# Kernel tuning notes

Hardware: AMD Instinct MI355X
Metric: run time of the kernel (lower is better)

The kernel has to match this reference:

```python
import jax, jax.numpy as jnp
import numpy as np

HEADS = 8
DIM_HEAD = 128
ATTN_MATRIX_SCALE = 1.5  # tau applied to mean-centered logits
SCALE = DIM_HEAD ** -0.5


def setup_inputs() -> dict:
    key = jax.random.key(0)
    ks = jax.random.split(key, 7)
    b, n, m = 2, 2048, 2048
    qd, cd, inner = 1024, 768, HEADS * DIM_HEAD
    x = jax.random.normal(ks[0], (b, n, qd), dtype=jnp.float32)
    context = jax.random.normal(ks[1], (b, m, cd), dtype=jnp.float32)
    Wq = jax.random.normal(ks[2], (qd, inner), dtype=jnp.float32) * (qd ** -0.5)
    Wk = jax.random.normal(ks[3], (cd, inner), dtype=jnp.float32) * (cd ** -0.5)
    Wv = jax.random.normal(ks[4], (cd, inner), dtype=jnp.float32) * (cd ** -0.5)
    Wout = jax.random.normal(ks[5], (inner, qd), dtype=jnp.float32) * (inner ** -0.5)
    bout = jnp.zeros((qd,), dtype=jnp.float32)
    return {"x": x, "context": context, "Wq": Wq, "Wk": Wk, "Wv": Wv,
            "Wout": Wout, "bout": bout}


def _split_heads(t):
    # (b, n, h*d) -> (h, b*n, d); matches rearrange '(b h) n d -> h (b n) d'
    b, n, _ = t.shape
    t = t.reshape(b, n, HEADS, DIM_HEAD)
    return t.transpose(2, 0, 1, 3).reshape(HEADS, b * n, DIM_HEAD)


def reference(x, context, Wq, Wk, Wv, Wout, bout):
    b, n, _ = x.shape
    qh = _split_heads(jnp.einsum('bnq,qi->bni', x, Wq))        # (h, b*n, d)
    kh = _split_heads(jnp.einsum('bmc,ci->bmi', context, Wk))  # (h, b*m, d)
    vh = _split_heads(jnp.einsum('bmc,ci->bmi', context, Wv))  # (h, b*m, d)

    # custom mean-centered / tau-scaled similarity (_compute_sim_with_tau)
    sim = jnp.einsum('hid,hjd->hij', qh, kh) * SCALE
    mean = jnp.mean(sim, axis=-1, keepdims=True)
    sim = (sim - mean) * ATTN_MATRIX_SCALE + mean

    attn = jax.nn.softmax(sim, axis=-1)
    out = jnp.einsum('hij,hjd->hid', attn, vh)                 # (h, b*n, d)

    # (h, b*n, d) -> (b, n, h*d)
    out = out.reshape(HEADS, b, n, DIM_HEAD).transpose(1, 2, 0, 3)
    out = out.reshape(b, n, HEADS * DIM_HEAD)
    return jnp.einsum('bni,iq->bnq', out, Wout) + bout
```

## Files before the change

### kernel.cpp

```cpp
#include <hip/hip_runtime.h>
#include <cstdint>
#include <cstddef>

typedef unsigned short u16t;
typedef __bf16 bf16x8_t __attribute__((ext_vector_type(8)));
typedef float f32x4_t __attribute__((ext_vector_type(4)));

#define MFMA_BF16 __builtin_amdgcn_mfma_f32_16x16x32_bf16

__device__ __forceinline__ u16t f2bf(float f) {
    uint32_t u = __builtin_bit_cast(uint32_t, f);
    u += 0x7fffu + ((u >> 16) & 1u);
    return (u16t)(u >> 16);
}

__device__ __forceinline__ uint32_t pk2bf(float a, float b) {
    return (uint32_t)f2bf(a) | ((uint32_t)f2bf(b) << 16);
}

__device__ __forceinline__ uint32_t pk2bf_fast(float a, float b) {
    uint32_t au = __builtin_bit_cast(uint32_t, a) + 0x8000u;
    uint32_t bu = __builtin_bit_cast(uint32_t, b) + 0x8000u;
    return __builtin_amdgcn_perm(bu, au, 0x07060302u);
}

__device__ __forceinline__ float bflo(uint32_t u) {
    return __builtin_bit_cast(float, u << 16);
}
__device__ __forceinline__ float bfhi(uint32_t u) {
    return __builtin_bit_cast(float, u & 0xffff0000u);
}

__device__ __forceinline__ bf16x8_t ld_frag(const u16t* p) {
    return __builtin_bit_cast(bf16x8_t, *(const uint4*)p);
}

__device__ __forceinline__ void gl_lds16(const u16t* g, u16t* l) {
    __builtin_amdgcn_global_load_lds(
        (const __attribute__((address_space(1))) void*)g,
        (__attribute__((address_space(3))) void*)l, 16, 0, 0);
}

__global__ void cast2_bf16_kernel(const float* __restrict__ s0, u16t* __restrict__ d0, int n0,
                                  const float* __restrict__ s1, u16t* __restrict__ d1, int n1) {
    int i = blockIdx.x * blockDim.x + threadIdx.x;
    const float* s; u16t* d;
    if (i < n0) { s = s0; d = d0; }
    else { i -= n0; if (i >= n1) return; s = s1; d = d1; }
    float4 v = ((const float4*)s)[i];
    uint2 o;
    o.x = pk2bf(v.x, v.y);
    o.y = pk2bf(v.z, v.w);
    ((uint2*)d)[i] = o;
}

__global__ void transpose4_kernel(const float* __restrict__ Wq, const float* __restrict__ Wk,
                                  const float* __restrict__ Wv, const float* __restrict__ Wo,
                                  u16t* __restrict__ Wqt, u16t* __restrict__ Wkt,
                                  u16t* __restrict__ Wvt, u16t* __restrict__ Wot) {
    const int z = blockIdx.z;
    const float* W = z == 0 ? Wq : (z == 1 ? Wk : (z == 2 ? Wv : Wo));
    u16t* Wt      = z == 0 ? Wqt : (z == 1 ? Wkt : (z == 2 ? Wvt : Wot));
    const int K   = (z == 1 || z == 2) ? 768 : 1024;
    const int N = 1024;
    int n0 = blockIdx.x * 32, k0 = blockIdx.y * 32;
    if (k0 >= K) return;
    __shared__ float tile[32][33];
    int tx = threadIdx.x, ty = threadIdx.y;
    for (int i = ty; i < 32; i += 8)
        tile[i][tx] = W[(size_t)(k0 + i) * N + n0 + tx];
    __syncthreads();
    for (int i = ty; i < 32; i += 8)
        Wt[(size_t)(n0 + i) * K + k0 + tx] = f2bf(tile[tx][i]);
}

__device__ __forceinline__ void gemm_core(
    const u16t* __restrict__ A, const u16t* __restrict__ Bt,
    int K, void* __restrict__ outp, const float* __restrict__ bias,
    int mode, float oscale, int bm, int bn)
{
    __shared__ __align__(16) u16t As[2][128 * 64];
    __shared__ __align__(16) u16t Bs[2][64 * 64];
    const int tid = threadIdx.x;
    const int wave = tid >> 6, lane = tid & 63;
    const int wm = wave & 1, wn = wave >> 1;
    const int quad = lane >> 4, l16 = lane & 15;

    const int l8r = lane >> 3, l8c = lane & 7;
    const int cgx = (l8c ^ l8r) * 8;

    f32x4_t acc[4][2];
#pragma unroll
    for (int i = 0; i < 4; ++i)
#pragma unroll
        for (int j = 0; j < 2; ++j) acc[i][j] = (f32x4_t){0.f, 0.f, 0.f, 0.f};

    const int nk = K >> 6;

#pragma unroll
    for (int it = 0; it < 4; ++it) {
        int rb = wave * 32 + it * 8;
        gl_lds16(&A[(size_t)(bm + rb + l8r) * K + cgx], &As[0][rb * 64]);
    }
#pragma unroll
    for (int it = 0; it < 2; ++it) {
        int rb = wave * 16 + it * 8;
        gl_lds16(&Bt[(size_t)(bn + rb + l8r) * K + cgx], &Bs[0][rb * 64]);
    }

    for (int ki = 0; ki < nk; ++ki) {
        const int buf = ki & 1;
        __syncthreads();

        if (ki + 1 < nk) {
            const int kc = (ki + 1) << 6;
#pragma unroll
            for (int it = 0; it < 4; ++it) {
                int rb = wave * 32 + it * 8;
                gl_lds16(&A[(size_t)(bm + rb + l8r) * K + kc + cgx], &As[buf ^ 1][rb * 64]);
            }
#pragma unroll
            for (int it = 0; it < 2; ++it) {
                int rb = wave * 16 + it * 8;
                gl_lds16(&Bt[(size_t)(bn + rb + l8r) * K + kc + cgx], &Bs[buf ^ 1][rb * 64]);
            }
        }

#pragma unroll
        for (int ks = 0; ks < 2; ++ks) {
            bf16x8_t af[4], bfv[2];
#pragma unroll
            for (int i = 0; i < 4; ++i) {
                int r = wm * 64 + i * 16 + l16;
                af[i] = ld_frag(&As[buf][r * 64 + (((ks * 4 + quad) ^ (r & 7)) * 8)]);
            }
#pragma unroll
            for (int j = 0; j < 2; ++j) {
                int r = wn * 32 + j * 16 + l16;
                bfv[j] = ld_frag(&Bs[buf][r * 64 + (((ks * 4 + quad) ^ (r & 7)) * 8)]);
            }
#pragma unroll
            for (int i = 0; i < 4; ++i)
#pragma unroll
                for (int j = 0; j < 2; ++j)
                    acc[i][j] = MFMA_BF16(af[i], bfv[j], acc[i][j], 0, 0, 0);
        }
    }

    if (mode == 3) {
        float* out = (float*)outp;
#pragma unroll
        for (int j = 0; j < 2; ++j) {
            int c = bn + wn * 32 + j * 16 + l16;
            float b = bias[c];
#pragma unroll
            for (int i = 0; i < 4; ++i) {
                int rb = bm + wm * 64 + i * 16 + quad * 4;
#pragma unroll
                for (int r = 0; r < 4; ++r)
                    out[(size_t)(rb + r) * 1024 + c] = acc[i][j][r] + b;
            }
        }
    } else if (mode == 2) {
        u16t* out = (u16t*)outp;
#pragma unroll
        for (int i = 0; i < 4; ++i)
#pragma unroll
            for (int j = 0; j < 2; ++j) {
                int rb = bm + wm * 64 + i * 16 + quad * 4;
                int c = bn + wn * 32 + j * 16 + l16;
                int h = c >> 7, d = c & 127;
                uint2 pk;
                pk.x = pk2bf(acc[i][j][0], acc[i][j][1]);
                pk.y = pk2bf(acc[i][j][2], acc[i][j][3]);
                *(uint2*)&out[((size_t)h * 128 + d) * 4096 + rb] = pk;
            }
    } else {
        u16t* out = (u16t*)outp;
#pragma unroll
        for (int i = 0; i < 4; ++i)
#pragma unroll
            for (int j = 0; j < 2; ++j) {
                int rb = bm + wm * 64 + i * 16 + quad * 4;
                int c = bn + wn * 32 + j * 16 + l16;
                int h = c >> 7, d = c & 127;
#pragma unroll
                for (int r = 0; r < 4; ++r)
                    out[((size_t)h * 4096 + rb + r) * 128 + d] = f2bf(acc[i][j][r] * oscale);
            }
    }
}

__global__ __launch_bounds__(256) void gemm_bf16_kernel(
    const u16t* __restrict__ A, const u16t* __restrict__ Bt,
    int K, void* __restrict__ outp, const float* __restrict__ bias,
    int mode, float oscale)
{
    gemm_core(A, Bt, K, outp, bias, mode, oscale, blockIdx.y * 128, blockIdx.x * 64);
}

__global__ __launch_bounds__(256) void qkv_kernel(
    const u16t* __restrict__ x_bf, const u16t* __restrict__ ctx_bf,
    const u16t* __restrict__ Wqt, const u16t* __restrict__ Wkt,
    const u16t* __restrict__ Wvt,
    u16t* __restrict__ Qh, u16t* __restrict__ Kh, u16t* __restrict__ Vt,
    float qscale)
{
    const int z = blockIdx.z;
    const u16t* A  = (z == 0) ? x_bf : ctx_bf;
    const u16t* Bt = (z == 0) ? Wqt : ((z == 1) ? Wkt : Wvt);
    void* outp     = (z == 0) ? (void*)Qh : ((z == 1) ? (void*)Kh : (void*)Vt);
    const int K    = (z == 0) ? 1024 : 768;
    const int mode = (z == 2) ? 2 : 0;
    const float sc = (z == 0) ? qscale : 1.0f;
    gemm_core(A, Bt, K, outp, nullptr, mode, sc, blockIdx.y * 128, blockIdx.x * 64);
}

__global__ __launch_bounds__(256) void flash_kernel(
    const u16t* __restrict__ Qh, const u16t* __restrict__ Kh,
    const u16t* __restrict__ Vtg, u16t* __restrict__ Op0,
    u16t* __restrict__ Op1, float* __restrict__ lp)
{
    extern __shared__ __align__(16) u16t smem[];
    u16t* Ps = smem + 16384;

    const int h = blockIdx.x;
    const int q0 = blockIdx.y * 64;
    const int z = blockIdx.z;
    const int tid = threadIdx.x;
    const int wave = tid >> 6, lane = tid & 63;
    const int quad = lane >> 4, l16 = lane & 15;

    const u16t* Kg = Kh + (size_t)h * 4096 * 128 + (size_t)z * 2048 * 128;
    const u16t* Vg = Vtg + (size_t)h * 128 * 4096 + z * 2048;

    {
        const u16t* Qg = Qh + ((size_t)h * 4096 + q0) * 128;
        const int sr = tid >> 4, c8 = tid & 15;
#pragma unroll
        for (int it = 0; it < 4; ++it) {
            int r = sr + it * 16;
            uint4 v = *(const uint4*)&Qg[r * 128 + c8 * 8];
            *(uint4*)&smem[r * 128 + ((c8 ^ (r & 15)) * 8)] = v;
        }
    }
    __syncthreads();
    bf16x8_t qf[4];
    {
        int r = wave * 16 + l16;
#pragma unroll
        for (int ks = 0; ks < 4; ++ks)
            qf[ks] = ld_frag(&smem[r * 128 + (((ks * 4 + quad) ^ (r & 15)) * 8)]);
    }
    __syncthreads();

    const int rK = lane >> 4, cK = lane & 15;
    const int rV = lane >> 2, cV = lane & 3;
    const bool kRole = wave < 2;
    const int wh = wave & 1;

    if (kRole) {
#pragma unroll
        for (int it = 0; it < 4; ++it) {
            int row = wh * 16 + it * 4 + rK;
            gl_lds16(Kg + (size_t)row * 128 + ((cK ^ (row & 15)) * 8),
                     smem + (wh * 16 + it * 4) * 128);
        }
    } else {
#pragma unroll
        for (int it = 0; it < 4; ++it) {
            int row = wh * 64 + it * 16 + rV;
            gl_lds16(Vg + (size_t)row * 4096 + ((cV ^ ((row >> 1) & 3)) * 8),
                     smem + 8192 + (wh * 64 + it * 16) * 32);
        }
    }

    f32x4_t O[8];
#pragma unroll
    for (int dt = 0; dt < 8; ++dt) O[dt] = (f32x4_t){0.f, 0.f, 0.f, 0.f};
    float lsum = 0.f;
    const int prow = wave * 16 + l16;
    const int psw = (prow >> 1) & 3;

    for (int kb = 0; kb < 64; ++kb) {
        const int bo  = (kb & 1) * 4096;
        const int bon = 4096 - bo;
        __syncthreads();

        if (kb < 63) {
            const int j0n = (kb + 1) * 32;
            if (kRole) {
#pragma unroll
                for (int it = 0; it < 4; ++it) {
                    int row = wh * 16 + it * 4 + rK;
                    gl_lds16(Kg + (size_t)(j0n + row) * 128 + ((cK ^ (row & 15)) * 8),
                             smem + bon + (wh * 16 + it * 4) * 128);
                }
            } else {
#pragma unroll
                for (int it = 0; it < 4; ++it) {
                    int row = wh * 64 + it * 16 + rV;
                    gl_lds16(Vg + (size_t)row * 4096 + j0n + ((cV ^ ((row >> 1) & 3)) * 8),
                             smem + 8192 + bon + (wh * 64 + it * 16) * 32);
                }
            }
        }

        const u16t* Ks = smem + bo;
        const u16t* Vs = smem + 8192 + bo;

        f32x4_t S[2];
#pragma unroll
        for (int jt = 0; jt < 2; ++jt) {
            S[jt] = (f32x4_t){0.f, 0.f, 0.f, 0.f};
            int rk = jt * 16 + l16;
#pragma unroll
            for (int ks = 0; ks < 4; ++ks) {
                bf16x8_t kf = ld_frag(&Ks[rk * 128 + (((ks * 4 + quad) ^ (rk & 15)) * 8)]);
                S[jt] = MFMA_BF16(kf, qf[ks], S[jt], 0, 0, 0);
            }
        }

#pragma unroll
        for (int jt = 0; jt < 2; ++jt) {
            float e0 = __builtin_amdgcn_exp2f(S[jt][0]);
            float e1 = __builtin_amdgcn_exp2f(S[jt][1]);
            float e2 = __builtin_amdgcn_exp2f(S[jt][2]);
            float e3 = __builtin_amdgcn_exp2f(S[jt][3]);
            lsum += (e0 + e1) + (e2 + e3);
            uint2 pk;
            pk.x = pk2bf_fast(e0, e1);
            pk.y = pk2bf_fast(e2, e3);
            int ch = (jt * 2 + (quad >> 1)) ^ psw;
            *(uint2*)&Ps[prow * 32 + ch * 8 + (quad & 1) * 4] = pk;
        }

        {
            bf16x8_t pf = ld_frag(&Ps[prow * 32 + ((quad ^ psw) * 8)]);
#pragma unroll
            for (int dt = 0; dt < 8; ++dt) {
                int rv = dt * 16 + l16;
                bf16x8_t vf = ld_frag(&Vs[rv * 32 + ((quad ^ ((rv >> 1) & 3)) * 8)]);
                O[dt] = MFMA_BF16(vf, pf, O[dt], 0, 0, 0);
            }
        }
    }

    lsum += __shfl_xor(lsum, 16, 64);
    lsum += __shfl_xor(lsum, 32, 64);
    u16t* Op = z ? Op1 : Op0;
    size_t i = (size_t)(q0 + wave * 16 + l16);
    if (quad == 0) lp[z * 32768 + i * 8 + h] = lsum;
#pragma unroll
    for (int dt = 0; dt < 8; ++dt) {
        uint2 pk;
        pk.x = pk2bf(O[dt][0], O[dt][1]);
        pk.y = pk2bf(O[dt][2], O[dt][3]);
        *(uint2*)&Op[i * 1024 + h * 128 + dt * 16 + quad * 4] = pk;
    }
}

__global__ __launch_bounds__(256) void combine_kernel(
    const u16t* __restrict__ O0, const u16t* __restrict__ O1,
    const float* __restrict__ lp, u16t* __restrict__ out)
{
    int t = blockIdx.x * blockDim.x + threadIdx.x;
    int e = t << 3;
    int i = e >> 10, h = (e >> 7) & 7;
    float inv = 1.f / (lp[i * 8 + h] + lp[32768 + i * 8 + h]);
    uint4 a = ((const uint4*)O0)[t];
    uint4 b = ((const uint4*)O1)[t];
    uint4 r;
    r.x = pk2bf((bflo(a.x) + bflo(b.x)) * inv, (bfhi(a.x) + bfhi(b.x)) * inv);
    r.y = pk2bf((bflo(a.y) + bflo(b.y)) * inv, (bfhi(a.y) + bfhi(b.y)) * inv);
    r.z = pk2bf((bflo(a.z) + bflo(b.z)) * inv, (bfhi(a.z) + bfhi(b.z)) * inv);
    r.w = pk2bf((bflo(a.w) + bflo(b.w)) * inv, (bfhi(a.w) + bfhi(b.w)) * inv);
    ((uint4*)out)[t] = r;
}

extern "C" void kernel_launch(void* const* d_in, const int* in_sizes, int n_in,
                              void* d_out, int out_size, void* d_ws, size_t ws_size,
                              hipStream_t stream)
{
    (void)in_sizes; (void)n_in; (void)out_size; (void)ws_size;
    const float* x    = (const float*)d_in[0];
    const float* ctx  = (const float*)d_in[1];
    const float* Wq   = (const float*)d_in[2];
    const float* Wk   = (const float*)d_in[3];
    const float* Wv   = (const float*)d_in[4];
    const float* Wout = (const float*)d_in[5];
    const float* bout = (const float*)d_in[6];
    float* out = (float*)d_out;

    u16t* ws = (u16t*)d_ws;
    u16t* x_bf   = ws;
    u16t* ctx_bf = x_bf + 4194304;
    u16t* Wqt    = ctx_bf + 3145728;
    u16t* Wkt    = Wqt + 1048576;
    u16t* Wvt    = Wkt + 786432;
    u16t* Woutt  = Wvt + 786432;
    u16t* Qh     = Woutt + 1048576;
    u16t* Kh     = Qh + 4194304;
    u16t* Vt     = Kh + 4194304;
    u16t* Oh   = x_bf;
    u16t* Ohp1 = ws + 4194304;
    float* lp  = (float*)(ws + 8388608);

    constexpr float QSCALE = 1.5f * 0.08838834764831845f * 1.4426950408889634f;

    (void)hipFuncSetAttribute((const void*)flash_kernel,
                              hipFuncAttributeMaxDynamicSharedMemorySize, 36864);

    cast2_bf16_kernel<<<7168, 256, 0, stream>>>(x, x_bf, 1048576, ctx, ctx_bf, 786432);
    transpose4_kernel<<<dim3(32, 32, 4), dim3(32, 8), 0, stream>>>(
        Wq, Wk, Wv, Wout, Wqt, Wkt, Wvt, Woutt);

    qkv_kernel<<<dim3(16, 32, 3), 256, 0, stream>>>(
        x_bf, ctx_bf, Wqt, Wkt, Wvt, Qh, Kh, Vt, QSCALE);

    flash_kernel<<<dim3(8, 64, 2), 256, 36864, stream>>>(Qh, Kh, Vt, Oh, Ohp1, lp);
    combine_kernel<<<4096, 256, 0, stream>>>(Oh, Ohp1, lp, Oh);

    gemm_bf16_kernel<<<dim3(16, 32), 256, 0, stream>>>(Oh, Woutt, 1024, out, bout, 3, 1.0f);
}
```

Before: 259.3 us.

## Retile projection GEMMs to 64-row tiles with K-step 32 and templated N width

Rewrites the shared GEMM core as a template over N width. Tiles become 64x128 for the QKV projection and 64x64 for the output projection, with a K step of 32 instead of 64. The XOR swizzle on the LDS fragment loads is dropped. More, smaller blocks raise occupancy and spread work across more CUs. In exchange, each block does fewer MFMAs per barrier, reuses less data, and the unswizzled 64-byte rows may cause LDS bank conflicts.

```diff
diff --git a/kernel.cpp b/kernel.cpp
--- a/kernel.cpp
+++ b/kernel.cpp
@@ -74,38 +74,37 @@
         Wt[(size_t)(n0 + i) * K + k0 + tx] = f2bf(tile[tx][i]);
 }
 
+template <int JN>
 __device__ __forceinline__ void gemm_core(
     const u16t* __restrict__ A, const u16t* __restrict__ Bt,
     int K, void* __restrict__ outp, const float* __restrict__ bias,
     int mode, float oscale, int bm, int bn)
 {
-    __shared__ __align__(16) u16t As[2][128 * 64];
-    __shared__ __align__(16) u16t Bs[2][64 * 64];
+    constexpr int BN = JN * 32;
+    __shared__ __align__(16) u16t As[2][64 * 32];
+    __shared__ __align__(16) u16t Bs[2][BN * 32];
     const int tid = threadIdx.x;
     const int wave = tid >> 6, lane = tid & 63;
     const int wm = wave & 1, wn = wave >> 1;
     const int quad = lane >> 4, l16 = lane & 15;
 
-    const int l8r = lane >> 3, l8c = lane & 7;
-    const int cgx = (l8c ^ l8r) * 8;
-
-    f32x4_t acc[4][2];
-#pragma unroll
-    for (int i = 0; i < 4; ++i)
-#pragma unroll
-        for (int j = 0; j < 2; ++j) acc[i][j] = (f32x4_t){0.f, 0.f, 0.f, 0.f};
-
-    const int nk = K >> 6;
-
-#pragma unroll
-    for (int it = 0; it < 4; ++it) {
-        int rb = wave * 32 + it * 8;
-        gl_lds16(&A[(size_t)(bm + rb + l8r) * K + cgx], &As[0][rb * 64]);
-    }
-#pragma unroll
-    for (int it = 0; it < 2; ++it) {
-        int rb = wave * 16 + it * 8;
-        gl_lds16(&Bt[(size_t)(bn + rb + l8r) * K + cgx], &Bs[0][rb * 64]);
+    const int dr = lane >> 2;
+    const int dc = (lane & 3) * 8;
+
+    f32x4_t acc[2][JN];
+#pragma unroll
+    for (int i = 0; i < 2; ++i)
+#pragma unroll
+        for (int j = 0; j < JN; ++j) acc[i][j] = (f32x4_t){0.f, 0.f, 0.f, 0.f};
+
+    const int nk = K >> 5;
+    const int ra = wave * 16;
+
+    gl_lds16(&A[(size_t)(bm + ra + dr) * K + dc], &As[0][ra * 32]);
+#pragma unroll
+    for (int it = 0; it < JN / 2; ++it) {
+        int rb = wave * (JN * 8) + it * 16;
+        gl_lds16(&Bt[(size_t)(bn + rb + dr) * K + dc], &Bs[0][rb * 32]);
     }
 
     for (int ki = 0; ki < nk; ++ki) {
@@ -113,49 +112,38 @@
         __syncthreads();
 
         if (ki + 1 < nk) {
-            const int kc = (ki + 1) << 6;
-#pragma unroll
-            for (int it = 0; it < 4; ++it) {
-                int rb = wave * 32 + it * 8;
-                gl_lds16(&A[(size_t)(bm + rb + l8r) * K + kc + cgx], &As[buf ^ 1][rb * 64]);
-            }
-#pragma unroll
-            for (int it = 0; it < 2; ++it) {
-                int rb = wave * 16 + it * 8;
-                gl_lds16(&Bt[(size_t)(bn + rb + l8r) * K + kc + cgx], &Bs[buf ^ 1][rb * 64]);
-            }
-        }
-
-#pragma unroll
-        for (int ks = 0; ks < 2; ++ks) {
-            bf16x8_t af[4], bfv[2];
-#pragma unroll
-            for (int i = 0; i < 4; ++i) {
-                int r = wm * 64 + i * 16 + l16;
-                af[i] = ld_frag(&As[buf][r * 64 + (((ks * 4 + quad) ^ (r & 7)) * 8)]);
-            }
-#pragma unroll
-            for (int j = 0; j < 2; ++j) {
-                int r = wn * 32 + j * 16 + l16;
-                bfv[j] = ld_frag(&Bs[buf][r * 64 + (((ks * 4 + quad) ^ (r & 7)) * 8)]);
-            }
-#pragma unroll
-            for (int i = 0; i < 4; ++i)
-#pragma unroll
-                for (int j = 0; j < 2; ++j)
-                    acc[i][j] = MFMA_BF16(af[i], bfv[j], acc[i][j], 0, 0, 0);
-        }
+            const int kc = (ki + 1) << 5;
+            gl_lds16(&A[(size_t)(bm + ra + dr) * K + kc + dc], &As[buf ^ 1][ra * 32]);
+#pragma unroll
+            for (int it = 0; it < JN / 2; ++it) {
+                int rb = wave * (JN * 8) + it * 16;
+                gl_lds16(&Bt[(size_t)(bn + rb + dr) * K + kc + dc], &Bs[buf ^ 1][rb * 32]);
+            }
+        }
+
+        bf16x8_t af[2], bfv[JN];
+#pragma unroll
+        for (int i = 0; i < 2; ++i)
+            af[i] = ld_frag(&As[buf][(wm * 32 + i * 16 + l16) * 32 + quad * 8]);
+#pragma unroll
+        for (int j = 0; j < JN; ++j)
+            bfv[j] = ld_frag(&Bs[buf][(wn * (JN * 16) + j * 16 + l16) * 32 + quad * 8]);
+#pragma unroll
+        for (int i = 0; i < 2; ++i)
+#pragma unroll
+            for (int j = 0; j < JN; ++j)
+                acc[i][j] = MFMA_BF16(af[i], bfv[j], acc[i][j], 0, 0, 0);
     }
 
     if (mode == 3) {
         float* out = (float*)outp;
 #pragma unroll
-        for (int j = 0; j < 2; ++j) {
-            int c = bn + wn * 32 + j * 16 + l16;
+        for (int j = 0; j < JN; ++j) {
+            int c = bn + wn * (JN * 16) + j * 16 + l16;
             float b = bias[c];
 #pragma unroll
-            for (int i = 0; i < 4; ++i) {
-                int rb = bm + wm * 64 + i * 16 + quad * 4;
+            for (int i = 0; i < 2; ++i) {
+                int rb = bm + wm * 32 + i * 16 + quad * 4;
 #pragma unroll
                 for (int r = 0; r < 4; ++r)
                     out[(size_t)(rb + r) * 1024 + c] = acc[i][j][r] + b;
@@ -164,11 +152,11 @@
     } else if (mode == 2) {
         u16t* out = (u16t*)outp;
 #pragma unroll
-        for (int i = 0; i < 4; ++i)
-#pragma unroll
-            for (int j = 0; j < 2; ++j) {
-                int rb = bm + wm * 64 + i * 16 + quad * 4;
-                int c = bn + wn * 32 + j * 16 + l16;
+        for (int i = 0; i < 2; ++i)
+#pragma unroll
+            for (int j = 0; j < JN; ++j) {
+                int rb = bm + wm * 32 + i * 16 + quad * 4;
+                int c = bn + wn * (JN * 16) + j * 16 + l16;
                 int h = c >> 7, d = c & 127;
                 uint2 pk;
                 pk.x = pk2bf(acc[i][j][0], acc[i][j][1]);
@@ -178,25 +166,17 @@
     } else {
         u16t* out = (u16t*)outp;
 #pragma unroll
-        for (int i = 0; i < 4; ++i)
-#pragma unroll
-            for (int j = 0; j < 2; ++j) {
-                int rb = bm + wm * 64 + i * 16 + quad * 4;
-                int c = bn + wn * 32 + j * 16 + l16;
+        for (int i = 0; i < 2; ++i)
+#pragma unroll
+            for (int j = 0; j < JN; ++j) {
+                int rb = bm + wm * 32 + i * 16 + quad * 4;
+                int c = bn + wn * (JN * 16) + j * 16 + l16;
                 int h = c >> 7, d = c & 127;
 #pragma unroll
                 for (int r = 0; r < 4; ++r)
                     out[((size_t)h * 4096 + rb + r) * 128 + d] = f2bf(acc[i][j][r] * oscale);
             }
     }
-}
-
-__global__ __launch_bounds__(256) void gemm_bf16_kernel(
-    const u16t* __restrict__ A, const u16t* __restrict__ Bt,
-    int K, void* __restrict__ outp, const float* __restrict__ bias,
-    int mode, float oscale)
-{
-    gemm_core(A, Bt, K, outp, bias, mode, oscale, blockIdx.y * 128, blockIdx.x * 64);
 }
 
 __global__ __launch_bounds__(256) void qkv_kernel(
@@ -213,7 +193,14 @@
     const int K    = (z == 0) ? 1024 : 768;
     const int mode = (z == 2) ? 2 : 0;
     const float sc = (z == 0) ? qscale : 1.0f;
-    gemm_core(A, Bt, K, outp, nullptr, mode, sc, blockIdx.y * 128, blockIdx.x * 64);
+    gemm_core<4>(A, Bt, K, outp, nullptr, mode, sc, blockIdx.y * 64, blockIdx.x * 128);
+}
+
+__global__ __launch_bounds__(256) void gemm_out_kernel(
+    const u16t* __restrict__ A, const u16t* __restrict__ Bt,
+    float* __restrict__ out, const float* __restrict__ bias)
+{
+    gemm_core<2>(A, Bt, 1024, (void*)out, bias, 3, 1.0f, blockIdx.y * 64, blockIdx.x * 64);
 }
 
 __global__ __launch_bounds__(256) void flash_kernel(
@@ -415,11 +402,11 @@
     transpose4_kernel<<<dim3(32, 32, 4), dim3(32, 8), 0, stream>>>(
         Wq, Wk, Wv, Wout, Wqt, Wkt, Wvt, Woutt);
 
-    qkv_kernel<<<dim3(16, 32, 3), 256, 0, stream>>>(
+    qkv_kernel<<<dim3(8, 64, 3), 256, 0, stream>>>(
         x_bf, ctx_bf, Wqt, Wkt, Wvt, Qh, Kh, Vt, QSCALE);
 
     flash_kernel<<<dim3(8, 64, 2), 256, 36864, stream>>>(Qh, Kh, Vt, Oh, Ohp1, lp);
     combine_kernel<<<4096, 256, 0, stream>>>(Oh, Ohp1, lp, Oh);
 
-    gemm_bf16_kernel<<<dim3(16, 32), 256, 0, stream>>>(Oh, Woutt, 1024, out, bout, 3, 1.0f);
-}
+    gemm_out_kernel<<<dim3(16, 64), 256, 0, stream>>>(Oh, Woutt, out, bout);
+}
```

Measured after the change: 271.3 us. 4.6% more time.
